# Performance work log

Measured on AMD Instinct MI355X. Metric: run time of the kernel, lower is better.

The kernel has to match this reference:

```python
import jax, jax.numpy as jnp
from jax import lax
import numpy as np

B, L, OBS_DIM, ACT_DIM = 4, 1024, 60, 2
D_MODEL, N_LAYERS, D_STATE, D_CONV, EXPAND = 256, 4, 16, 4, 2
D_INNER = EXPAND * D_MODEL
DT_RANK = (D_MODEL + 15) // 16  # mamba_ssm default: ceil(d_model/16)


def setup_inputs() -> dict:
    key = jax.random.key(0)
    ks = jax.random.split(key, 12)
    rn = lambda k, s, sc: jax.random.normal(k, s, jnp.float32) * sc
    return {
        "obs_seq": jax.random.normal(ks[0], (B, L, OBS_DIM), jnp.float32),
        "input_proj_w": rn(ks[1], (D_MODEL, OBS_DIM), OBS_DIM ** -0.5),
        "input_proj_b": jnp.zeros((D_MODEL,), jnp.float32),
        "norm_w": jnp.ones((N_LAYERS, D_MODEL), jnp.float32),
        "norm_b": jnp.zeros((N_LAYERS, D_MODEL), jnp.float32),
        "in_proj_w": rn(ks[2], (N_LAYERS, 2 * D_INNER, D_MODEL), D_MODEL ** -0.5),
        "conv_w": rn(ks[3], (N_LAYERS, D_INNER, D_CONV), D_CONV ** -0.5),
        "conv_b": jnp.zeros((N_LAYERS, D_INNER), jnp.float32),
        "x_proj_w": rn(ks[4], (N_LAYERS, DT_RANK + 2 * D_STATE, D_INNER), D_INNER ** -0.5),
        "dt_proj_w": rn(ks[5], (N_LAYERS, D_INNER, DT_RANK), DT_RANK ** -0.5),
        "dt_proj_b": jnp.full((N_LAYERS, D_INNER), float(np.log(np.expm1(0.01))), jnp.float32),
        "A_log": jnp.log(jnp.broadcast_to(jnp.arange(1, D_STATE + 1, dtype=jnp.float32), (N_LAYERS, D_INNER, D_STATE))),
        "D_skip": jnp.ones((N_LAYERS, D_INNER), jnp.float32),
        "out_proj_w": rn(ks[6], (N_LAYERS, D_MODEL, D_INNER), D_INNER ** -0.5),
        "policy_mean_w": rn(ks[7], (ACT_DIM, D_MODEL), 0.01 * D_MODEL ** -0.5),
        "policy_mean_b": jnp.zeros((ACT_DIM,), jnp.float32),
        "policy_log_std": jnp.zeros((ACT_DIM,), jnp.float32),
        "value_w": rn(ks[8], (1, D_MODEL), D_MODEL ** -0.5),
        "value_b": jnp.zeros((1,), jnp.float32),
    }


def _silu(x):
    return x * jax.nn.sigmoid(x)


def _layer_norm(x, w, b):
    m = jnp.mean(x, -1, keepdims=True)
    v = jnp.mean(jnp.square(x - m), -1, keepdims=True)
    return (x - m) * lax.rsqrt(v + 1e-5) * w + b


def _mamba(x, in_w, cw, cb, xw, dtw, dtb, a_log, d_skip, ow):
    # x: (B, L, d_model)
    xz = jnp.einsum('bld,ed->ble', x, in_w)            # (B, L, 2*d_inner)
    xi, z = xz[..., :D_INNER], xz[..., D_INNER:]
    # depthwise causal conv, width D_CONV
    xp = jnp.pad(xi, ((0, 0), (D_CONV - 1, 0), (0, 0)))
    conv = sum(xp[:, k:k + L, :] * cw[:, k] for k in range(D_CONV)) + cb
    xi = _silu(conv)
    dbc = jnp.einsum('bld,ed->ble', xi, xw)            # (B, L, dt_rank + 2*d_state)
    dt = jax.nn.softplus(jnp.einsum('blr,dr->bld', dbc[..., :DT_RANK], dtw) + dtb)
    Bm = dbc[..., DT_RANK:DT_RANK + D_STATE]           # (B, L, N)
    Cm = dbc[..., DT_RANK + D_STATE:]                  # (B, L, N)
    A = -jnp.exp(a_log)                                # (d_inner, N)
    dA = jnp.exp(dt[..., None] * A)                    # (B, L, d_inner, N)
    dBx = (dt * xi)[..., None] * Bm[:, :, None, :]     # (B, L, d_inner, N)

    def comb(c1, c2):
        a1, b1 = c1
        a2, b2 = c2
        return a2 * a1, a2 * b1 + b2

    _, h = lax.associative_scan(comb, (dA, dBx), axis=1)  # h_t = dA_t*h_{t-1} + dBx_t
    y = jnp.einsum('bldn,bln->bld', h, Cm) + d_skip * xi
    return jnp.einsum('bld,ed->ble', y * _silu(z), ow)


def _forward(obs_seq, input_proj_w, input_proj_b, norm_w, norm_b, in_proj_w, conv_w,
             conv_b, x_proj_w, dt_proj_w, dt_proj_b, A_log, D_skip, out_proj_w,
             policy_mean_w, policy_mean_b, policy_log_std, value_w, value_b):
    x = _silu(jnp.einsum('blo,do->bld', obs_seq, input_proj_w) + input_proj_b)
    for i in range(N_LAYERS):  # pre-norm residual Mamba blocks
        x = x + _mamba(_layer_norm(x, norm_w[i], norm_b[i]), in_proj_w[i], conv_w[i],
                       conv_b[i], x_proj_w[i], dt_proj_w[i], dt_proj_b[i], A_log[i],
                       D_skip[i], out_proj_w[i])
    mu = jnp.einsum('bld,ad->bla', x, policy_mean_w) + policy_mean_b
    std = jnp.broadcast_to(jnp.exp(policy_log_std), mu.shape)
    value = jnp.einsum('bld,od->blo', x, value_w) + value_b
    return mu, std, value


def reference(obs_seq, input_proj_w, input_proj_b, norm_w, norm_b, in_proj_w, conv_w,
              conv_b, x_proj_w, dt_proj_w, dt_proj_b, A_log, D_skip, out_proj_w,
              policy_mean_w, policy_mean_b, policy_log_std, value_w, value_b):
    return _forward(obs_seq, input_proj_w, input_proj_b, norm_w, norm_b, in_proj_w,
                    conv_w, conv_b, x_proj_w, dt_proj_w, dt_proj_b, A_log, D_skip,
                    out_proj_w, policy_mean_w, policy_mean_b, policy_log_std,
                    value_w, value_b)
```

## Files before the change

kernel.cpp:

```cpp
#include <hip/hip_runtime.h>
#include <hip/hip_bf16.h>

#define Bsz 4
#define Lseq 1024
#define OBS 60
#define DM 256
#define DI 512
#define DTR 16
#define DST 16
#define NTOK (Bsz*Lseq)
#define NCH 64
#define CH  16

typedef _Float16 half8 __attribute__((ext_vector_type(8)));
typedef float floatx4 __attribute__((ext_vector_type(4)));

__device__ __forceinline__ float silu_f(float v) {
    return v * (1.f / (1.f + __expf(-v)));
}
__device__ __forceinline__ float softplus_f(float v) {
    return fmaxf(v, 0.f) + log1pf(__expf(-fabsf(v)));
}

__device__ __forceinline__ void compute_dA(float dtv, const float* An,
                                           bool structured, float* dA) {
    if (structured) {
        float p1 = __expf(-dtv);
        float p2 = p1*p1, p4 = p2*p2, p8 = p4*p4;
        dA[0]=p1;      dA[1]=p2;      dA[2]=p2*p1;    dA[3]=p4;
        dA[4]=p4*p1;   dA[5]=p4*p2;   dA[6]=p4*dA[2]; dA[7]=p8;
        dA[8]=p8*p1;   dA[9]=p8*p2;   dA[10]=p8*dA[2];dA[11]=p8*p4;
        dA[12]=p8*dA[4];dA[13]=p8*dA[5];dA[14]=p8*dA[6];dA[15]=p8*p8;
    } else {
        #pragma unroll
        for (int n = 0; n < 16; ++n) dA[n] = __expf(dtv*An[n]);
    }
}

#define NIN_W  (4*1024*256)
#define NX_W   (4*64*512)
#define NOUT_W (4*256*512)
__global__ __launch_bounds__(256) void convert_weights(
    const float* __restrict__ inw, const float* __restrict__ xw,
    const float* __restrict__ ow, _Float16* __restrict__ wh_in,
    _Float16* __restrict__ wh_x, _Float16* __restrict__ wh_out) {
    int idx = blockIdx.x*256 + threadIdx.x;
    if (idx < NIN_W) {
        wh_in[idx] = (_Float16)inw[idx];
    } else if (idx < NIN_W + NX_W) {
        int r = idx - NIN_W;
        int layer = r >> 15;
        int rem = r & 32767;
        int n = rem >> 9, k = rem & 511;
        wh_x[r] = (_Float16)((n < 48) ? xw[((size_t)layer*48 + n)*512 + k] : 0.f);
    } else if (idx < NIN_W + NX_W + NOUT_W) {
        int r = idx - NIN_W - NX_W;
        wh_out[r] = (_Float16)ow[r];
    }
}

__global__ __launch_bounds__(256) void input_proj_ln(
    const float* __restrict__ obs, const float* __restrict__ W,
    const float* __restrict__ bias, const float* __restrict__ nw,
    const float* __restrict__ nb, float* __restrict__ x,
    _Float16* __restrict__ xn_h) {
    int t = blockIdx.x; int tid = threadIdx.x;
    __shared__ float so[OBS];
    if (tid < OBS) so[tid] = obs[t*OBS + tid];
    __syncthreads();
    float acc = bias[tid];
    const float* wr = W + tid*OBS;
    #pragma unroll
    for (int k = 0; k < OBS; ++k) acc += so[k]*wr[k];
    float v = silu_f(acc);
    x[t*DM + tid] = v;
    float s = v;
    #pragma unroll
    for (int off = 32; off; off >>= 1) s += __shfl_down(s, off);
    __shared__ float ps[4];
    __shared__ float mean_s, rstd_s;
    int wid = tid >> 6, lane = tid & 63;
    if (lane == 0) ps[wid] = s;
    __syncthreads();
    if (tid == 0) mean_s = (ps[0]+ps[1]+ps[2]+ps[3]) * (1.f/DM);
    __syncthreads();
    float m = mean_s;
    float d = v - m;
    float sq = d*d;
    #pragma unroll
    for (int off = 32; off; off >>= 1) sq += __shfl_down(sq, off);
    if (lane == 0) ps[wid] = sq;
    __syncthreads();
    if (tid == 0) rstd_s = rsqrtf((ps[0]+ps[1]+ps[2]+ps[3])*(1.f/DM) + 1e-5f);
    __syncthreads();
    xn_h[t*DM + tid] = (_Float16)(d * rstd_s * nw[tid] + nb[tid]);
}

template<int BM, int BN, int WM, int WN, int EPI>
__global__ __launch_bounds__(256) void hgemm_nt(
    const _Float16* __restrict__ A, const _Float16* __restrict__ W,
    void* __restrict__ Cout, const float* __restrict__ resid,
    int M, int N, int K, int ldc,
    const float* __restrict__ e0, const float* __restrict__ e1,
    const float* __restrict__ e2, const float* __restrict__ e3,
    const float* __restrict__ e4,
    float* __restrict__ xout, _Float16* __restrict__ xnh) {
    constexpr int MFR = BM/(WM*16);
    constexpr int NFR = BN/(WN*16);
    __shared__ _Float16 As[BM*64];
    __shared__ _Float16 Bs[BN*64];
    int tid = threadIdx.x;
    int r0 = blockIdx.y*BM, c0 = blockIdx.x*BN;
    int w = tid >> 6, lane = tid & 63;
    int wr = w / WN, wc = w % WN;
    floatx4 acc[MFR][NFR];
    #pragma unroll
    for (int i = 0; i < MFR; ++i)
        #pragma unroll
        for (int j = 0; j < NFR; ++j)
            acc[i][j] = (floatx4)0.f;

    for (int k0 = 0; k0 < K; k0 += 64) {
        #pragma unroll
        for (int c = 0; c < BM/32; ++c) {
            int q = tid + 256*c;
            int row = q >> 3, cc = (q & 7)*8;
            half8 v = *(const half8*)&A[(size_t)(r0 + row)*K + k0 + cc];
            *(half8*)&As[row*64 + (cc ^ ((row & 7) << 3))] = v;
        }
        #pragma unroll
        for (int c = 0; c < BN/32; ++c) {
            int q = tid + 256*c;
            int row = q >> 3, cc = (q & 7)*8;
            half8 v = *(const half8*)&W[(size_t)(c0 + row)*K + k0 + cc];
            *(half8*)&Bs[row*64 + (cc ^ ((row & 7) << 3))] = v;
        }
        __syncthreads();
        #pragma unroll
        for (int kc = 0; kc < 2; ++kc) {
            half8 a[MFR], b[NFR];
            int col = kc*32 + (lane >> 4)*8;
            #pragma unroll
            for (int i = 0; i < MFR; ++i) {
                int row = wr*(BM/WM) + i*16 + (lane & 15);
                a[i] = *(const half8*)&As[row*64 + (col ^ ((row & 7) << 3))];
            }
            #pragma unroll
            for (int j = 0; j < NFR; ++j) {
                int row = wc*(BN/WN) + j*16 + (lane & 15);
                b[j] = *(const half8*)&Bs[row*64 + (col ^ ((row & 7) << 3))];
            }
            #pragma unroll
            for (int i = 0; i < MFR; ++i)
                #pragma unroll
                for (int j = 0; j < NFR; ++j)
                    acc[i][j] = __builtin_amdgcn_mfma_f32_16x16x32_f16(a[i], b[j], acc[i][j], 0, 0, 0);
        }
        __syncthreads();
    }
    if constexpr (EPI == 0) {
        float* C = (float*)Cout;
        #pragma unroll
        for (int i = 0; i < MFR; ++i) {
            int m0 = r0 + wr*(BM/WM) + i*16 + (lane >> 4)*4;
            #pragma unroll
            for (int j = 0; j < NFR; ++j) {
                int col = c0 + wc*(BN/WN) + j*16 + (lane & 15);
                if (col < N) {
                    #pragma unroll
                    for (int t = 0; t < 4; ++t)
                        C[(size_t)(m0 + t)*ldc + col] = acc[i][j][t];
                }
            }
        }
    } else if constexpr (EPI == 1) {
        _Float16* C = (_Float16*)Cout;
        #pragma unroll
        for (int i = 0; i < MFR; ++i) {
            int m0 = r0 + wr*(BM/WM) + i*16 + (lane >> 4)*4;
            #pragma unroll
            for (int j = 0; j < NFR; ++j) {
                int col = c0 + wc*(BN/WN) + j*16 + (lane & 15);
                #pragma unroll
                for (int t = 0; t < 4; ++t)
                    C[(size_t)(m0 + t)*ldc + col] = (_Float16)acc[i][j][t];
            }
        }
    } else {
        int g = lane >> 4, ln16 = lane & 15;
        #pragma unroll
        for (int t = 0; t < 4; ++t) {
            int row = r0 + wr*16 + g*4 + t;
            #pragma unroll
            for (int j = 0; j < NFR; ++j)
                acc[0][j][t] += resid[(size_t)row*DM + j*16 + ln16];
        }
        if constexpr (EPI == 2) {
            #pragma unroll
            for (int t = 0; t < 4; ++t) {
                int row = r0 + wr*16 + g*4 + t;
                float s = 0.f, sq = 0.f;
                #pragma unroll
                for (int j = 0; j < NFR; ++j) {
                    float v = acc[0][j][t];
                    xout[(size_t)row*DM + j*16 + ln16] = v;
                    s += v; sq += v*v;
                }
                #pragma unroll
                for (int msk = 1; msk < 16; msk <<= 1) {
                    s += __shfl_xor(s, msk);
                    sq += __shfl_xor(sq, msk);
                }
                float mean = s * (1.f/DM);
                float rstd = rsqrtf(sq*(1.f/DM) - mean*mean + 1e-5f);
                #pragma unroll
                for (int j = 0; j < NFR; ++j) {
                    int col = j*16 + ln16;
                    float v = acc[0][j][t];
                    xnh[(size_t)row*DM + col] =
                        (_Float16)((v - mean)*rstd*e0[col] + e1[col]);
                }
            }
        } else {
            float* out = xout;
            #pragma unroll
            for (int t = 0; t < 4; ++t) {
                int row = r0 + wr*16 + g*4 + t;
                float m0 = 0.f, m1 = 0.f, vv = 0.f;
                #pragma unroll
                for (int j = 0; j < NFR; ++j) {
                    int col = j*16 + ln16;
                    float v = acc[0][j][t];
                    m0 += v*e0[col]; m1 += v*e0[DM + col]; vv += v*e3[col];
                }
                #pragma unroll
                for (int msk = 1; msk < 16; msk <<= 1) {
                    m0 += __shfl_xor(m0, msk);
                    m1 += __shfl_xor(m1, msk);
                    vv += __shfl_xor(vv, msk);
                }
                if (ln16 == 0) {
                    out[row*2 + 0] = m0 + e1[0];
                    out[row*2 + 1] = m1 + e1[1];
                    out[2*NTOK + row*2 + 0] = __expf(e2[0]);
                    out[2*NTOK + row*2 + 1] = __expf(e2[1]);
                    out[4*NTOK + row] = vv + e4[0];
                }
            }
        }
    }
}

__global__ __launch_bounds__(256) void conv_silu_kernel(
    const _Float16* __restrict__ xz_h, const float* __restrict__ cw,
    const float* __restrict__ cb, _Float16* __restrict__ xi_h) {
    int idx = blockIdx.x*blockDim.x + threadIdx.x;
    if (idx >= NTOK*DI) return;
    int d = idx & (DI-1); int t = idx >> 9;
    int l = t & (Lseq-1); int b = t >> 10;
    float acc = cb[d];
    #pragma unroll
    for (int k = 0; k < 4; ++k) {
        int ls = l - 3 + k;
        if (ls >= 0) acc += (float)xz_h[((size_t)(b*Lseq + ls))*(2*DI) + d] * cw[d*4 + k];
    }
    xi_h[idx] = (_Float16)silu_f(acc);
}

__global__ __launch_bounds__(256) void scan_phaseA(
    const _Float16* __restrict__ xi_h, const float* __restrict__ dbc,
    const float* __restrict__ dtw, const float* __restrict__ dtb,
    const float* __restrict__ a_log, float* __restrict__ Ap,
    float* __restrict__ He) {
    __shared__ float sdbc[CH*48];
    int blk = blockIdx.x;
    int b = blk >> 7; int rem = blk & 127; int c = rem >> 1; int half = rem & 1;
    int d = half*256 + threadIdx.x;
    const float* src = dbc + ((size_t)(b*Lseq + c*CH))*48;
    for (int q = threadIdx.x; q < CH*48; q += 256) sdbc[q] = src[q];
    float wreg[16];
    #pragma unroll
    for (int r = 0; r < DTR; ++r) wreg[r] = dtw[d*DTR + r];
    float bias = dtb[d];
    float An[16];
    bool structured = true;
    #pragma unroll
    for (int n = 0; n < 16; ++n) {
        An[n] = -__expf(a_log[d*16 + n]);
        structured = structured && (fabsf(An[n] + (float)(n+1)) < 1e-4f*(n+1));
    }
    __syncthreads();
    float h[16] = {};
    float ap[16];
    #pragma unroll
    for (int n = 0; n < 16; ++n) ap[n] = 1.f;
    for (int s = 0; s < CH; ++s) {
        int t = b*Lseq + c*CH + s;
        float xiv = (float)xi_h[(size_t)t*DI + d];
        float dl = bias;
        #pragma unroll
        for (int r = 0; r < DTR; ++r) dl += sdbc[s*48 + r]*wreg[r];
        float dtv = softplus_f(dl);
        float u = dtv*xiv;
        float dA[16];
        compute_dA(dtv, An, structured, dA);
        #pragma unroll
        for (int n = 0; n < 16; ++n) {
            h[n] = dA[n]*h[n] + u*sdbc[s*48 + DTR + n];
            ap[n] *= dA[n];
        }
    }
    size_t base = ((size_t)(b*NCH + c)*16)*DI + d;
    #pragma unroll
    for (int n = 0; n < 16; ++n) { Ap[base + n*DI] = ap[n]; He[base + n*DI] = h[n]; }
}

__global__ __launch_bounds__(256) void scan_phaseB(
    const float* __restrict__ Ap, const float* __restrict__ He,
    float* __restrict__ h0) {
    int g = blockIdx.x*blockDim.x + threadIdx.x;
    int b = g >> 13; int n = (g >> 9) & 15; int d = g & 511;
    float run = 0.f;
    for (int c = 0; c < NCH; ++c) {
        size_t idx = ((size_t)(b*NCH + c)*16 + n)*DI + d;
        float a = Ap[idx], e = He[idx];
        h0[idx] = run;
        run = a*run + e;
    }
}

__global__ __launch_bounds__(256) void scan_phaseC(
    const _Float16* __restrict__ xi_h, const float* __restrict__ dbc,
    const float* __restrict__ dtw, const float* __restrict__ dtb,
    const float* __restrict__ a_log, const float* __restrict__ dskip,
    const _Float16* __restrict__ xz_h, const float* __restrict__ h0,
    _Float16* __restrict__ yg_h) {
    __shared__ float sdbc[CH*48];
    int blk = blockIdx.x;
    int b = blk >> 7; int rem = blk & 127; int c = rem >> 1; int half = rem & 1;
    int d = half*256 + threadIdx.x;
    const float* src = dbc + ((size_t)(b*Lseq + c*CH))*48;
    for (int q = threadIdx.x; q < CH*48; q += 256) sdbc[q] = src[q];
    float wreg[16];
    #pragma unroll
    for (int r = 0; r < DTR; ++r) wreg[r] = dtw[d*DTR + r];
    float bias = dtb[d];
    float An[16];
    bool structured = true;
    #pragma unroll
    for (int n = 0; n < 16; ++n) {
        An[n] = -__expf(a_log[d*16 + n]);
        structured = structured && (fabsf(An[n] + (float)(n+1)) < 1e-4f*(n+1));
    }
    __syncthreads();
    float h[16];
    size_t base = ((size_t)(b*NCH + c)*16)*DI + d;
    #pragma unroll
    for (int n = 0; n < 16; ++n) h[n] = h0[base + n*DI];
    float ds = dskip[d];
    for (int s = 0; s < CH; ++s) {
        int t = b*Lseq + c*CH + s;
        float xiv = (float)xi_h[(size_t)t*DI + d];
        float dl = bias;
        #pragma unroll
        for (int r = 0; r < DTR; ++r) dl += sdbc[s*48 + r]*wreg[r];
        float dtv = softplus_f(dl);
        float u = dtv*xiv;
        float dA[16];
        compute_dA(dtv, An, structured, dA);
        float y = ds*xiv;
        #pragma unroll
        for (int n = 0; n < 16; ++n) {
            h[n] = dA[n]*h[n] + u*sdbc[s*48 + DTR + n];
            y += h[n]*sdbc[s*48 + DTR + DST + n];
        }
        float zv = (float)xz_h[(size_t)t*(2*DI) + DI + d];
        yg_h[(size_t)t*DI + d] = (_Float16)(y * silu_f(zv));
    }
}

extern "C" void kernel_launch(void* const* d_in, const int* in_sizes, int n_in,
                              void* d_out, int out_size, void* d_ws, size_t ws_size,
                              hipStream_t stream) {
    const float* obs = (const float*)d_in[0];
    const float* ipw = (const float*)d_in[1];
    const float* ipb = (const float*)d_in[2];
    const float* nw  = (const float*)d_in[3];
    const float* nb  = (const float*)d_in[4];
    const float* inw = (const float*)d_in[5];
    const float* cw  = (const float*)d_in[6];
    const float* cb  = (const float*)d_in[7];
    const float* xw  = (const float*)d_in[8];
    const float* dtw = (const float*)d_in[9];
    const float* dtb = (const float*)d_in[10];
    const float* alog= (const float*)d_in[11];
    const float* dsk = (const float*)d_in[12];
    const float* ow  = (const float*)d_in[13];
    const float* pw  = (const float*)d_in[14];
    const float* pb  = (const float*)d_in[15];
    const float* ls  = (const float*)d_in[16];
    const float* vw  = (const float*)d_in[17];
    const float* vb  = (const float*)d_in[18];
    float* out = (float*)d_out;

    float* ws = (float*)d_ws;
    float* x   = ws;
    float* dbc = x   + 1048576;
    float* Ap  = dbc + 196608;
    float* He  = Ap  + 2097152;
    float* h0  = Ap;
    _Float16* f16b  = (_Float16*)(He + 2097152);
    _Float16* xz_h  = f16b;
    _Float16* xn_h  = xz_h  + 4194304;
    _Float16* xi_h  = xn_h  + 1048576;
    _Float16* yg_h  = xi_h  + 2097152;
    _Float16* wh_in = yg_h  + 2097152;
    _Float16* wh_x  = wh_in + 1048576;
    _Float16* wh_out= wh_x  + 131072;

    convert_weights<<<(NIN_W + NX_W + NOUT_W + 255)/256, 256, 0, stream>>>(
        inw, xw, ow, wh_in, wh_x, wh_out);
    input_proj_ln<<<NTOK, 256, 0, stream>>>(obs, ipw, ipb, nw, nb, x, xn_h);

    for (int i = 0; i < 4; ++i) {
        {
            dim3 g(1024/64, NTOK/128);
            hgemm_nt<128,64,2,2,1><<<g, 256, 0, stream>>>(
                xn_h, wh_in + (size_t)i*1024*256, xz_h, nullptr, NTOK, 1024, 256, 1024,
                nullptr, nullptr, nullptr, nullptr, nullptr, nullptr, nullptr);
        }
        conv_silu_kernel<<<(NTOK*DI)/256, 256, 0, stream>>>(xz_h, cw + i*DI*4, cb + i*DI, xi_h);
        {
            dim3 g(1, NTOK/32);
            hgemm_nt<32,64,2,2,0><<<g, 256, 0, stream>>>(
                xi_h, wh_x + (size_t)i*64*512, dbc, nullptr, NTOK, 48, 512, 48,
                nullptr, nullptr, nullptr, nullptr, nullptr, nullptr, nullptr);
        }
        scan_phaseA<<<Bsz*NCH*2, 256, 0, stream>>>(
            xi_h, dbc, dtw + (size_t)i*DI*DTR, dtb + i*DI,
            alog + (size_t)i*DI*DST, Ap, He);
        scan_phaseB<<<128, 256, 0, stream>>>(Ap, He, h0);
        scan_phaseC<<<Bsz*NCH*2, 256, 0, stream>>>(
            xi_h, dbc, dtw + (size_t)i*DI*DTR, dtb + i*DI,
            alog + (size_t)i*DI*DST, dsk + i*DI, xz_h, h0, yg_h);
        {
            dim3 g(1, NTOK/64);
            if (i < 3) {
                hgemm_nt<64,256,4,1,2><<<g, 256, 0, stream>>>(
                    yg_h, wh_out + (size_t)i*256*512, nullptr, x, NTOK, 256, 512, 256,
                    nw + (i+1)*DM, nb + (i+1)*DM, nullptr, nullptr, nullptr, x, xn_h);
            } else {
                hgemm_nt<64,256,4,1,3><<<g, 256, 0, stream>>>(
                    yg_h, wh_out + (size_t)i*256*512, nullptr, x, NTOK, 256, 512, 256,
                    pw, pb, ls, vw, vb, out, nullptr);
            }
        }
    }
}
```

Before: 373.0 us.

## Fuse causal conv into x_proj GEMM and scan, store scan carries in fp16

Removes the standalone conv+SiLU kernel. A new GEMM kernel recomputes the depthwise conv and SiLU while loading its A tile from xz, and scan phase A recomputes the conv on the fly, writing xi and dt for phase C. Phase C then reads dt instead of recomputing the dt projection and softplus. The chunk carry buffers (Ap, He, h0) move from fp32 to fp16 to halve their traffic, which risks precision loss in the inter-chunk state propagation, especially for He and h0.

```diff
diff --git a/kernel.cpp b/kernel.cpp
--- a/kernel.cpp
+++ b/kernel.cpp
@@ -40,10 +40,12 @@
 #define NIN_W  (4*1024*256)
 #define NX_W   (4*64*512)
 #define NOUT_W (4*256*512)
+#define NCWT   (4*4*512)
 __global__ __launch_bounds__(256) void convert_weights(
     const float* __restrict__ inw, const float* __restrict__ xw,
-    const float* __restrict__ ow, _Float16* __restrict__ wh_in,
-    _Float16* __restrict__ wh_x, _Float16* __restrict__ wh_out) {
+    const float* __restrict__ ow, const float* __restrict__ cw,
+    _Float16* __restrict__ wh_in, _Float16* __restrict__ wh_x,
+    _Float16* __restrict__ wh_out, _Float16* __restrict__ cwT) {
     int idx = blockIdx.x*256 + threadIdx.x;
     if (idx < NIN_W) {
         wh_in[idx] = (_Float16)inw[idx];
@@ -56,6 +58,12 @@
     } else if (idx < NIN_W + NX_W + NOUT_W) {
         int r = idx - NIN_W - NX_W;
         wh_out[r] = (_Float16)ow[r];
+    } else if (idx < NIN_W + NX_W + NOUT_W + NCWT) {
+        int r = idx - NIN_W - NX_W - NOUT_W;
+        int layer = r >> 11;
+        int rem = r & 2047;
+        int k = rem >> 9, d = rem & 511;
+        cwT[r] = (_Float16)cw[layer*2048 + d*4 + k];
     }
 }
 
@@ -158,35 +166,20 @@
         }
         __syncthreads();
     }
-    if constexpr (EPI == 0) {
-        float* C = (float*)Cout;
+    if constexpr (EPI == 1) {
+        _Float16* C = (_Float16*)Cout;
         #pragma unroll
         for (int i = 0; i < MFR; ++i) {
             int m0 = r0 + wr*(BM/WM) + i*16 + (lane >> 4)*4;
             #pragma unroll
             for (int j = 0; j < NFR; ++j) {
                 int col = c0 + wc*(BN/WN) + j*16 + (lane & 15);
-                if (col < N) {
-                    #pragma unroll
-                    for (int t = 0; t < 4; ++t)
-                        C[(size_t)(m0 + t)*ldc + col] = acc[i][j][t];
-                }
-            }
-        }
-    } else if constexpr (EPI == 1) {
-        _Float16* C = (_Float16*)Cout;
-        #pragma unroll
-        for (int i = 0; i < MFR; ++i) {
-            int m0 = r0 + wr*(BM/WM) + i*16 + (lane >> 4)*4;
-            #pragma unroll
-            for (int j = 0; j < NFR; ++j) {
-                int col = c0 + wc*(BN/WN) + j*16 + (lane & 15);
                 #pragma unroll
                 for (int t = 0; t < 4; ++t)
                     C[(size_t)(m0 + t)*ldc + col] = (_Float16)acc[i][j][t];
             }
         }
-    } else {
+    } else if constexpr (EPI == 2 || EPI == 3) {
         int g = lane >> 4, ln16 = lane & 15;
         #pragma unroll
         for (int t = 0; t < 4; ++t) {
@@ -251,27 +244,86 @@
     }
 }
 
-__global__ __launch_bounds__(256) void conv_silu_kernel(
-    const _Float16* __restrict__ xz_h, const float* __restrict__ cw,
-    const float* __restrict__ cb, _Float16* __restrict__ xi_h) {
-    int idx = blockIdx.x*blockDim.x + threadIdx.x;
-    if (idx >= NTOK*DI) return;
-    int d = idx & (DI-1); int t = idx >> 9;
-    int l = t & (Lseq-1); int b = t >> 10;
-    float acc = cb[d];
-    #pragma unroll
-    for (int k = 0; k < 4; ++k) {
-        int ls = l - 3 + k;
-        if (ls >= 0) acc += (float)xz_h[((size_t)(b*Lseq + ls))*(2*DI) + d] * cw[d*4 + k];
-    }
-    xi_h[idx] = (_Float16)silu_f(acc);
+__global__ __launch_bounds__(256) void xproj_conv_gemm(
+    const _Float16* __restrict__ xz_h, const _Float16* __restrict__ Wx,
+    const _Float16* __restrict__ cwT, const float* __restrict__ cb,
+    float* __restrict__ dbc) {
+    __shared__ _Float16 As[32*64];
+    __shared__ _Float16 Bs[64*64];
+    int tid = threadIdx.x;
+    int r0 = blockIdx.x*32;
+    int w = tid >> 6, lane = tid & 63;
+    int wr = w >> 1, wc = w & 1;
+    floatx4 acc[2];
+    acc[0] = (floatx4)0.f; acc[1] = (floatx4)0.f;
+    for (int k0 = 0; k0 < 512; k0 += 64) {
+        {
+            int row = tid >> 3, e8 = tid & 7;
+            int d = k0 + e8*8;
+            int t = r0 + row, l = t & (Lseq-1);
+            half8 zero8;
+            zero8 = (half8)((_Float16)0.f);
+            half8 v0 = (l >= 3) ? *(const half8*)&xz_h[(size_t)(t-3)*1024 + d] : zero8;
+            half8 v1 = (l >= 2) ? *(const half8*)&xz_h[(size_t)(t-2)*1024 + d] : zero8;
+            half8 v2 = (l >= 1) ? *(const half8*)&xz_h[(size_t)(t-1)*1024 + d] : zero8;
+            half8 v3 = *(const half8*)&xz_h[(size_t)t*1024 + d];
+            half8 c0 = *(const half8*)&cwT[0*512 + d];
+            half8 c1 = *(const half8*)&cwT[1*512 + d];
+            half8 c2 = *(const half8*)&cwT[2*512 + d];
+            half8 c3 = *(const half8*)&cwT[3*512 + d];
+            half8 o;
+            #pragma unroll
+            for (int e = 0; e < 8; ++e) {
+                float a = cb[d + e];
+                a += (float)v0[e]*(float)c0[e];
+                a += (float)v1[e]*(float)c1[e];
+                a += (float)v2[e]*(float)c2[e];
+                a += (float)v3[e]*(float)c3[e];
+                o[e] = (_Float16)silu_f(a);
+            }
+            *(half8*)&As[row*64 + ((e8*8) ^ ((row & 7) << 3))] = o;
+        }
+        #pragma unroll
+        for (int c = 0; c < 2; ++c) {
+            int q = tid + 256*c;
+            int row = q >> 3, cc = (q & 7)*8;
+            half8 vv = *(const half8*)&Wx[(size_t)row*512 + k0 + cc];
+            *(half8*)&Bs[row*64 + (cc ^ ((row & 7) << 3))] = vv;
+        }
+        __syncthreads();
+        #pragma unroll
+        for (int kc = 0; kc < 2; ++kc) {
+            int col = kc*32 + (lane >> 4)*8;
+            int arow = wr*16 + (lane & 15);
+            half8 a = *(const half8*)&As[arow*64 + (col ^ ((arow & 7) << 3))];
+            #pragma unroll
+            for (int j = 0; j < 2; ++j) {
+                int brow = wc*32 + j*16 + (lane & 15);
+                half8 b = *(const half8*)&Bs[brow*64 + (col ^ ((brow & 7) << 3))];
+                acc[j] = __builtin_amdgcn_mfma_f32_16x16x32_f16(a, b, acc[j], 0, 0, 0);
+            }
+        }
+        __syncthreads();
+    }
+    int m0 = r0 + wr*16 + (lane >> 4)*4;
+    #pragma unroll
+    for (int j = 0; j < 2; ++j) {
+        int col = wc*32 + j*16 + (lane & 15);
+        if (col < 48) {
+            #pragma unroll
+            for (int t = 0; t < 4; ++t)
+                dbc[(size_t)(m0 + t)*48 + col] = acc[j][t];
+        }
+    }
 }
 
 __global__ __launch_bounds__(256) void scan_phaseA(
-    const _Float16* __restrict__ xi_h, const float* __restrict__ dbc,
+    const _Float16* __restrict__ xz_h, const float* __restrict__ dbc,
     const float* __restrict__ dtw, const float* __restrict__ dtb,
-    const float* __restrict__ a_log, float* __restrict__ Ap,
-    float* __restrict__ He) {
+    const float* __restrict__ a_log, const float* __restrict__ cw,
+    const float* __restrict__ cb,
+    _Float16* __restrict__ xi_h, _Float16* __restrict__ dt_h,
+    _Float16* __restrict__ Ap, _Float16* __restrict__ He) {
     __shared__ float sdbc[CH*48];
     int blk = blockIdx.x;
     int b = blk >> 7; int rem = blk & 127; int c = rem >> 1; int half = rem & 1;
@@ -282,6 +334,8 @@
     #pragma unroll
     for (int r = 0; r < DTR; ++r) wreg[r] = dtw[d*DTR + r];
     float bias = dtb[d];
+    float4 cwv = *(const float4*)&cw[d*4];
+    float cbv = cb[d];
     float An[16];
     bool structured = true;
     #pragma unroll
@@ -289,18 +343,30 @@
         An[n] = -__expf(a_log[d*16 + n]);
         structured = structured && (fabsf(An[n] + (float)(n+1)) < 1e-4f*(n+1));
     }
+    int l0 = c*CH; int t0 = b*Lseq + l0;
+    float w0 = 0.f, w1 = 0.f, w2 = 0.f;
+    if (l0 >= 3) {
+        w0 = (float)xz_h[(size_t)(t0-3)*1024 + d];
+        w1 = (float)xz_h[(size_t)(t0-2)*1024 + d];
+        w2 = (float)xz_h[(size_t)(t0-1)*1024 + d];
+    }
     __syncthreads();
     float h[16] = {};
     float ap[16];
     #pragma unroll
     for (int n = 0; n < 16; ++n) ap[n] = 1.f;
     for (int s = 0; s < CH; ++s) {
-        int t = b*Lseq + c*CH + s;
-        float xiv = (float)xi_h[(size_t)t*DI + d];
+        float cur = (float)xz_h[(size_t)(t0+s)*1024 + d];
+        float conv = cbv + cwv.x*w0 + cwv.y*w1 + cwv.z*w2 + cwv.w*cur;
+        w0 = w1; w1 = w2; w2 = cur;
+        float xiv = silu_f(conv);
         float dl = bias;
         #pragma unroll
         for (int r = 0; r < DTR; ++r) dl += sdbc[s*48 + r]*wreg[r];
         float dtv = softplus_f(dl);
+        size_t ti = (size_t)(t0+s)*DI + d;
+        xi_h[ti] = (_Float16)xiv;
+        dt_h[ti] = (_Float16)dtv;
         float u = dtv*xiv;
         float dA[16];
         compute_dA(dtv, An, structured, dA);
@@ -312,39 +378,37 @@
     }
     size_t base = ((size_t)(b*NCH + c)*16)*DI + d;
     #pragma unroll
-    for (int n = 0; n < 16; ++n) { Ap[base + n*DI] = ap[n]; He[base + n*DI] = h[n]; }
+    for (int n = 0; n < 16; ++n) {
+        Ap[base + n*DI] = (_Float16)ap[n];
+        He[base + n*DI] = (_Float16)h[n];
+    }
 }
 
 __global__ __launch_bounds__(256) void scan_phaseB(
-    const float* __restrict__ Ap, const float* __restrict__ He,
-    float* __restrict__ h0) {
+    const _Float16* __restrict__ Ap, const _Float16* __restrict__ He,
+    _Float16* __restrict__ h0) {
     int g = blockIdx.x*blockDim.x + threadIdx.x;
     int b = g >> 13; int n = (g >> 9) & 15; int d = g & 511;
     float run = 0.f;
     for (int c = 0; c < NCH; ++c) {
         size_t idx = ((size_t)(b*NCH + c)*16 + n)*DI + d;
-        float a = Ap[idx], e = He[idx];
-        h0[idx] = run;
+        float a = (float)Ap[idx], e = (float)He[idx];
+        h0[idx] = (_Float16)run;
         run = a*run + e;
     }
 }
 
 __global__ __launch_bounds__(256) void scan_phaseC(
-    const _Float16* __restrict__ xi_h, const float* __restrict__ dbc,
-    const float* __restrict__ dtw, const float* __restrict__ dtb,
-    const float* __restrict__ a_log, const float* __restrict__ dskip,
-    const _Float16* __restrict__ xz_h, const float* __restrict__ h0,
-    _Float16* __restrict__ yg_h) {
+    const _Float16* __restrict__ xi_h, const _Float16* __restrict__ dt_h,
+    const float* __restrict__ dbc, const float* __restrict__ a_log,
+    const float* __restrict__ dskip, const _Float16* __restrict__ xz_h,
+    const _Float16* __restrict__ h0, _Float16* __restrict__ yg_h) {
     __shared__ float sdbc[CH*48];
     int blk = blockIdx.x;
     int b = blk >> 7; int rem = blk & 127; int c = rem >> 1; int half = rem & 1;
     int d = half*256 + threadIdx.x;
     const float* src = dbc + ((size_t)(b*Lseq + c*CH))*48;
     for (int q = threadIdx.x; q < CH*48; q += 256) sdbc[q] = src[q];
-    float wreg[16];
-    #pragma unroll
-    for (int r = 0; r < DTR; ++r) wreg[r] = dtw[d*DTR + r];
-    float bias = dtb[d];
     float An[16];
     bool structured = true;
     #pragma unroll
@@ -353,18 +417,16 @@
         structured = structured && (fabsf(An[n] + (float)(n+1)) < 1e-4f*(n+1));
     }
     __syncthreads();
+    int t0 = b*Lseq + c*CH;
     float h[16];
     size_t base = ((size_t)(b*NCH + c)*16)*DI + d;
     #pragma unroll
-    for (int n = 0; n < 16; ++n) h[n] = h0[base + n*DI];
+    for (int n = 0; n < 16; ++n) h[n] = (float)h0[base + n*DI];
     float ds = dskip[d];
     for (int s = 0; s < CH; ++s) {
-        int t = b*Lseq + c*CH + s;
-        float xiv = (float)xi_h[(size_t)t*DI + d];
-        float dl = bias;
-        #pragma unroll
-        for (int r = 0; r < DTR; ++r) dl += sdbc[s*48 + r]*wreg[r];
-        float dtv = softplus_f(dl);
+        size_t ti = (size_t)(t0+s)*DI + d;
+        float xiv = (float)xi_h[ti];
+        float dtv = (float)dt_h[ti];
         float u = dtv*xiv;
         float dA[16];
         compute_dA(dtv, An, structured, dA);
@@ -374,8 +436,8 @@
             h[n] = dA[n]*h[n] + u*sdbc[s*48 + DTR + n];
             y += h[n]*sdbc[s*48 + DTR + DST + n];
         }
-        float zv = (float)xz_h[(size_t)t*(2*DI) + DI + d];
-        yg_h[(size_t)t*DI + d] = (_Float16)(y * silu_f(zv));
+        float zv = (float)xz_h[(size_t)(t0+s)*1024 + DI + d];
+        yg_h[ti] = (_Float16)(y * silu_f(zv));
     }
 }
 
@@ -406,20 +468,22 @@
     float* ws = (float*)d_ws;
     float* x   = ws;
     float* dbc = x   + 1048576;
-    float* Ap  = dbc + 196608;
-    float* He  = Ap  + 2097152;
-    float* h0  = Ap;
-    _Float16* f16b  = (_Float16*)(He + 2097152);
+    _Float16* f16b  = (_Float16*)(dbc + 196608);
     _Float16* xz_h  = f16b;
     _Float16* xn_h  = xz_h  + 4194304;
     _Float16* xi_h  = xn_h  + 1048576;
-    _Float16* yg_h  = xi_h  + 2097152;
-    _Float16* wh_in = yg_h  + 2097152;
+    _Float16* dt_h  = xi_h  + 2097152;
+    _Float16* yg_h  = dt_h  + 2097152;
+    _Float16* Ap_h  = yg_h  + 2097152;
+    _Float16* He_h  = Ap_h  + 2097152;
+    _Float16* h0_h  = Ap_h;
+    _Float16* wh_in = He_h  + 2097152;
     _Float16* wh_x  = wh_in + 1048576;
     _Float16* wh_out= wh_x  + 131072;
-
-    convert_weights<<<(NIN_W + NX_W + NOUT_W + 255)/256, 256, 0, stream>>>(
-        inw, xw, ow, wh_in, wh_x, wh_out);
+    _Float16* cwT_h = wh_out+ 524288;
+
+    convert_weights<<<(NIN_W + NX_W + NOUT_W + NCWT + 255)/256, 256, 0, stream>>>(
+        inw, xw, ow, cw, wh_in, wh_x, wh_out, cwT_h);
     input_proj_ln<<<NTOK, 256, 0, stream>>>(obs, ipw, ipb, nw, nb, x, xn_h);
 
     for (int i = 0; i < 4; ++i) {
@@ -429,20 +493,16 @@
                 xn_h, wh_in + (size_t)i*1024*256, xz_h, nullptr, NTOK, 1024, 256, 1024,
                 nullptr, nullptr, nullptr, nullptr, nullptr, nullptr, nullptr);
         }
-        conv_silu_kernel<<<(NTOK*DI)/256, 256, 0, stream>>>(xz_h, cw + i*DI*4, cb + i*DI, xi_h);
-        {
-            dim3 g(1, NTOK/32);
-            hgemm_nt<32,64,2,2,0><<<g, 256, 0, stream>>>(
-                xi_h, wh_x + (size_t)i*64*512, dbc, nullptr, NTOK, 48, 512, 48,
-                nullptr, nullptr, nullptr, nullptr, nullptr, nullptr, nullptr);
-        }
+        xproj_conv_gemm<<<NTOK/32, 256, 0, stream>>>(
+            xz_h, wh_x + (size_t)i*64*512, cwT_h + i*2048, cb + i*DI, dbc);
         scan_phaseA<<<Bsz*NCH*2, 256, 0, stream>>>(
-            xi_h, dbc, dtw + (size_t)i*DI*DTR, dtb + i*DI,
-            alog + (size_t)i*DI*DST, Ap, He);
-        scan_phaseB<<<128, 256, 0, stream>>>(Ap, He, h0);
+            xz_h, dbc, dtw + (size_t)i*DI*DTR, dtb + i*DI,
+            alog + (size_t)i*DI*DST, cw + (size_t)i*DI*4, cb + i*DI,
+            xi_h, dt_h, Ap_h, He_h);
+        scan_phaseB<<<128, 256, 0, stream>>>(Ap_h, He_h, h0_h);
         scan_phaseC<<<Bsz*NCH*2, 256, 0, stream>>>(
-            xi_h, dbc, dtw + (size_t)i*DI*DTR, dtb + i*DI,
-            alog + (size_t)i*DI*DST, dsk + i*DI, xz_h, h0, yg_h);
+            xi_h, dt_h, dbc, alog + (size_t)i*DI*DST,
+            dsk + i*DI, xz_h, h0_h, yg_h);
         {
             dim3 g(1, NTOK/64);
             if (i < 3) {
```

Result: faster. 336.5 us (-9.8%).
